# Optimization experiments

Hardware: AMD Instinct MI355X
Metric: run time of the kernel (lower is better)

The kernel has to match this reference:

```python
import jax, jax.numpy as jnp
import numpy as np

N = 50000      # nodes
E = 800000     # edges
D_IN = 512
D_OUT = 512
EDGE_DIM = 3


def setup_inputs() -> dict:
    key = jax.random.key(0)
    k = jax.random.split(key, 6)
    x = jax.random.normal(k[0], (N, D_IN), dtype=jnp.float32)
    edge_index = jax.random.randint(k[1], (2, E), 0, N, dtype=jnp.int64)
    edge_attr = jax.random.normal(k[2], (E, EDGE_DIM), dtype=jnp.float32)
    # xavier-uniform-ish init for linear weights
    lim1 = (6.0 / (D_IN + D_OUT)) ** 0.5
    lin_w = jax.random.uniform(k[3], (D_OUT, D_IN), minval=-lim1, maxval=lim1, dtype=jnp.float32)
    lin_b = jnp.zeros((D_OUT,), dtype=jnp.float32)
    lim2 = (6.0 / (EDGE_DIM + 1)) ** 0.5
    conf_w = jax.random.uniform(k[4], (1, EDGE_DIM), minval=-lim2, maxval=lim2, dtype=jnp.float32)
    conf_b = jnp.zeros((1,), dtype=jnp.float32)
    return {"x": x, "edge_index": edge_index, "edge_attr": edge_attr,
            "lin_w": lin_w, "lin_b": lin_b, "conf_w": conf_w, "conf_b": conf_b}


def reference(x, edge_index, edge_attr, lin_w, lin_b, conf_w, conf_b):
    row, col = edge_index[0], edge_index[1]
    # edge confidence weight: sigmoid(conf_lin(edge_attr)) -> [E]
    edge_weight = jax.nn.sigmoid(edge_attr @ conf_w.T + conf_b)[:, 0]
    # degree of source nodes (count of row occurrences), inverse sqrt with inf/nan -> 0
    deg = jnp.zeros((x.shape[0],), dtype=x.dtype).at[row].add(1.0)
    deg_safe = jnp.where(deg > 0, deg, 1.0)
    deg_inv_sqrt = jnp.where(deg > 0, jax.lax.rsqrt(deg_safe), 0.0)
    norm = deg_inv_sqrt[row] * deg_inv_sqrt[col] * edge_weight  # [E]
    norm = jnp.where(jnp.isnan(norm), 0.0, norm)
    # gather-scale-scatter: out[col] += x[row] * norm
    out = jnp.zeros_like(x).at[col].add(x[row] * norm[:, None])
    return out @ lin_w.T + lin_b
```

## Files before the change

### kernel.cpp

```cpp
#include <hip/hip_runtime.h>

#define NDIM 512

typedef __bf16 bf16x8 __attribute__((ext_vector_type(8)));
typedef float  f32x4  __attribute__((ext_vector_type(4)));

__device__ inline ushort f2bf(float f) {
    uint b = __float_as_uint(f);
    return (ushort)((b + 0x7fffu + ((b >> 16) & 1u)) >> 16);
}
__device__ inline float bflo(uint u) { return __uint_as_float(u << 16); }
__device__ inline float bfhi(uint u) { return __uint_as_float(u & 0xffff0000u); }
__device__ inline uint packbf(float lo, float hi) {
    return ((uint)f2bf(hi) << 16) | (uint)f2bf(lo);
}

__device__ inline void gload16(const ushort* g, ushort* l) {
    __builtin_amdgcn_global_load_lds(
        (const __attribute__((address_space(1))) uint*)g,
        (__attribute__((address_space(3))) uint*)l, 16, 0, 0);
}

__global__ __launch_bounds__(256) void f2bf_kernel(const float* __restrict__ in,
                                                   ushort* __restrict__ out, int n4) {
    int i = blockIdx.x * 256 + threadIdx.x;
    if (i >= n4) return;
    float4 v = ((const float4*)in)[i];
    ushort4 o;
    o.x = f2bf(v.x); o.y = f2bf(v.y); o.z = f2bf(v.z); o.w = f2bf(v.w);
    ((ushort4*)out)[i] = o;
}

__global__ __launch_bounds__(256) void hist_kernel(const int* __restrict__ ei,
                                                   int* __restrict__ deg_row,
                                                   int* __restrict__ cnt_col, int E) {
    int e = blockIdx.x * 256 + threadIdx.x;
    if (e < E) {
        atomicAdd(&deg_row[ei[e]], 1);
        atomicAdd(&cnt_col[ei[E + e]], 1);
    }
}

__global__ __launch_bounds__(256) void rsqrt_kernel(const int* __restrict__ deg,
                                                    float* __restrict__ dis, int n) {
    int i = blockIdx.x * 256 + threadIdx.x;
    if (i < n) {
        int d = deg[i];
        dis[i] = (d > 0) ? rsqrtf((float)d) : 0.0f;
    }
}

__global__ __launch_bounds__(1024) void scan_kernel(const int* __restrict__ cnt,
                                                    int* __restrict__ base, int n) {
    __shared__ int wsum[16];
    __shared__ int carry_s;
    int tid = threadIdx.x;
    int lane = tid & 63, wid = tid >> 6;
    if (tid == 0) carry_s = 0;
    __syncthreads();
    for (int s = 0; s < n; s += 4096) {
        int i0 = s + tid * 4;
        int v0 = 0, v1 = 0, v2 = 0, v3 = 0;
        if (i0 + 3 < n) {
            int4 q = *(const int4*)(cnt + i0);
            v0 = q.x; v1 = q.y; v2 = q.z; v3 = q.w;
        } else if (i0 < n) {
            v0 = cnt[i0];
            if (i0 + 1 < n) v1 = cnt[i0 + 1];
            if (i0 + 2 < n) v2 = cnt[i0 + 2];
        }
        int tsum = v0 + v1 + v2 + v3;
        int incl = tsum;
#pragma unroll
        for (int off = 1; off < 64; off <<= 1) {
            int t = __shfl_up(incl, off, 64);
            if (lane >= off) incl += t;
        }
        if (lane == 63) wsum[wid] = incl;
        __syncthreads();
        int add = carry_s;
#pragma unroll
        for (int w = 0; w < 16; ++w) if (w < wid) add += wsum[w];
        int run = add + incl - tsum;
        if (i0 + 0 < n) base[i0 + 0] = run; run += v0;
        if (i0 + 1 < n) base[i0 + 1] = run; run += v1;
        if (i0 + 2 < n) base[i0 + 2] = run; run += v2;
        if (i0 + 3 < n) base[i0 + 3] = run;
        __syncthreads();
        if (tid == 1023) carry_s = add + incl;
        __syncthreads();
    }
    if (tid == 0) base[n] = carry_s;
}

__global__ __launch_bounds__(256) void fill_kernel(
        const int* __restrict__ ei, const float* __restrict__ ea,
        const float* __restrict__ dis,
        const float* __restrict__ conf_w, const float* __restrict__ conf_b,
        const int* __restrict__ base, int* __restrict__ fill_cnt,
        int2* __restrict__ rn_sorted, int E) {
    int e = blockIdx.x * 256 + threadIdx.x;
    if (e >= E) return;
    int row = ei[e];
    int col = ei[E + e];
    float w = ea[(size_t)e*3+0]*conf_w[0] + ea[(size_t)e*3+1]*conf_w[1]
            + ea[(size_t)e*3+2]*conf_w[2] + conf_b[0];
    w = 1.0f / (1.0f + __expf(-w));
    float nm = dis[row] * dis[col] * w;
    int pos = base[col] + atomicAdd(&fill_cnt[col], 1);
    rn_sorted[pos] = make_int2(row, __float_as_int(nm));
}

__global__ __launch_bounds__(256) void agg_kernel(
        const ushort* __restrict__ xh, const int2* __restrict__ rn,
        const int* __restrict__ base, ushort* __restrict__ aggh, int N) {
    int wid  = threadIdx.x >> 6;
    int lane = threadIdx.x & 63;
    int node = blockIdx.x * 4 + wid;
    if (node >= N) return;
    int start = base[node], end = base[node + 1];
    const ushort* xc = xh + lane * 8;
    float a0 = 0.f, a1 = 0.f, a2 = 0.f, a3 = 0.f;
    float a4 = 0.f, a5 = 0.f, a6 = 0.f, a7 = 0.f;
    int p = start;
    for (; p + 4 <= end; p += 4) {
        int2 e0 = rn[p + 0];
        int2 e1 = rn[p + 1];
        int2 e2 = rn[p + 2];
        int2 e3 = rn[p + 3];
        uint4 u0 = *(const uint4*)(xc + ((size_t)e0.x << 9));
        uint4 u1 = *(const uint4*)(xc + ((size_t)e1.x << 9));
        uint4 u2 = *(const uint4*)(xc + ((size_t)e2.x << 9));
        uint4 u3 = *(const uint4*)(xc + ((size_t)e3.x << 9));
        float n0 = __int_as_float(e0.y);
        float n1 = __int_as_float(e1.y);
        float n2 = __int_as_float(e2.y);
        float n3 = __int_as_float(e3.y);
        a0 = fmaf(bflo(u0.x), n0, a0); a1 = fmaf(bfhi(u0.x), n0, a1);
        a2 = fmaf(bflo(u0.y), n0, a2); a3 = fmaf(bfhi(u0.y), n0, a3);
        a4 = fmaf(bflo(u0.z), n0, a4); a5 = fmaf(bfhi(u0.z), n0, a5);
        a6 = fmaf(bflo(u0.w), n0, a6); a7 = fmaf(bfhi(u0.w), n0, a7);
        a0 = fmaf(bflo(u1.x), n1, a0); a1 = fmaf(bfhi(u1.x), n1, a1);
        a2 = fmaf(bflo(u1.y), n1, a2); a3 = fmaf(bfhi(u1.y), n1, a3);
        a4 = fmaf(bflo(u1.z), n1, a4); a5 = fmaf(bfhi(u1.z), n1, a5);
        a6 = fmaf(bflo(u1.w), n1, a6); a7 = fmaf(bfhi(u1.w), n1, a7);
        a0 = fmaf(bflo(u2.x), n2, a0); a1 = fmaf(bfhi(u2.x), n2, a1);
        a2 = fmaf(bflo(u2.y), n2, a2); a3 = fmaf(bfhi(u2.y), n2, a3);
        a4 = fmaf(bflo(u2.z), n2, a4); a5 = fmaf(bfhi(u2.z), n2, a5);
        a6 = fmaf(bflo(u2.w), n2, a6); a7 = fmaf(bfhi(u2.w), n2, a7);
        a0 = fmaf(bflo(u3.x), n3, a0); a1 = fmaf(bfhi(u3.x), n3, a1);
        a2 = fmaf(bflo(u3.y), n3, a2); a3 = fmaf(bfhi(u3.y), n3, a3);
        a4 = fmaf(bflo(u3.z), n3, a4); a5 = fmaf(bfhi(u3.z), n3, a5);
        a6 = fmaf(bflo(u3.w), n3, a6); a7 = fmaf(bfhi(u3.w), n3, a7);
    }
    for (; p < end; ++p) {
        int2 e = rn[p];
        uint4 u = *(const uint4*)(xc + ((size_t)e.x << 9));
        float nm = __int_as_float(e.y);
        a0 = fmaf(bflo(u.x), nm, a0); a1 = fmaf(bfhi(u.x), nm, a1);
        a2 = fmaf(bflo(u.y), nm, a2); a3 = fmaf(bfhi(u.y), nm, a3);
        a4 = fmaf(bflo(u.z), nm, a4); a5 = fmaf(bfhi(u.z), nm, a5);
        a6 = fmaf(bflo(u.w), nm, a6); a7 = fmaf(bfhi(u.w), nm, a7);
    }
    uint4 o;
    o.x = packbf(a0, a1);
    o.y = packbf(a2, a3);
    o.z = packbf(a4, a5);
    o.w = packbf(a6, a7);
    *(uint4*)(aggh + (size_t)node * NDIM + lane * 8) = o;
}

__global__ __launch_bounds__(256) void mfma_gemm(
        const ushort* __restrict__ A,
        const ushort* __restrict__ B,
        const float* __restrict__ bias,
        float* __restrict__ out, int M) {
    __shared__ ushort As[128 * 32];
    __shared__ ushort Bs[128 * 32];
    int m0 = blockIdx.x * 128;
    int n0 = blockIdx.y * 128;
    int tid  = threadIdx.x;
    int lane = tid & 63;
    int wave = tid >> 6;
    int wr = wave >> 1, wc = wave & 1;
    int quad = lane >> 4, l16 = lane & 15;
    int lrow = lane >> 2, lcol = (lane & 3) << 3;

    f32x4 acc[4][4] = {};

    for (int k0 = 0; k0 < NDIM; k0 += 32) {
#pragma unroll
        for (int i = 0; i < 2; ++i) {
            int ch = wave * 2 + i;
            int r  = ch * 16 + lrow;
            int gm = m0 + r; if (gm >= M) gm = M - 1;
            gload16(A + ((size_t)gm << 9) + k0 + lcol, &As[ch * 512]);
            gload16(B + ((size_t)(n0 + r) << 9) + k0 + lcol, &Bs[ch * 512]);
        }
        __syncthreads();
#pragma unroll
        for (int mt = 0; mt < 4; ++mt) {
            bf16x8 a = *(const bf16x8*)&As[(wr * 64 + mt * 16 + l16) * 32 + quad * 8];
#pragma unroll
            for (int nt = 0; nt < 4; ++nt) {
                bf16x8 b = *(const bf16x8*)&Bs[(wc * 64 + nt * 16 + l16) * 32 + quad * 8];
                acc[mt][nt] = __builtin_amdgcn_mfma_f32_16x16x32_bf16(a, b, acc[mt][nt], 0, 0, 0);
            }
        }
        __syncthreads();
    }
#pragma unroll
    for (int mt = 0; mt < 4; ++mt) {
#pragma unroll
        for (int nt = 0; nt < 4; ++nt) {
            int gn = n0 + wc * 64 + nt * 16 + l16;
            float bv = bias[gn];
#pragma unroll
            for (int r = 0; r < 4; ++r) {
                int gm = m0 + wr * 64 + mt * 16 + quad * 4 + r;
                if (gm < M) out[(size_t)gm * NDIM + gn] = acc[mt][nt][r] + bv;
            }
        }
    }
}

extern "C" void kernel_launch(void* const* d_in, const int* in_sizes, int n_in,
                              void* d_out, int out_size, void* d_ws, size_t ws_size,
                              hipStream_t stream) {
    const float* x      = (const float*)d_in[0];
    const int*   ei     = (const int*)  d_in[1];
    const float* ea     = (const float*)d_in[2];
    const float* lin_w  = (const float*)d_in[3];
    const float* lin_b  = (const float*)d_in[4];
    const float* conf_w = (const float*)d_in[5];
    const float* conf_b = (const float*)d_in[6];
    float* out = (float*)d_out;

    int N = in_sizes[0] / NDIM;
    int E = in_sizes[2] / 3;

    char* p = (char*)d_ws;
    auto alloc = [&](size_t bytes) {
        char* q = p;
        p += (bytes + 255) & ~(size_t)255;
        return q;
    };
    ushort* aggh       = (ushort*)alloc((size_t)N * NDIM * sizeof(ushort));
    ushort* wh         = (ushort*)alloc((size_t)NDIM * NDIM * sizeof(ushort));
    int*   deg_row     = (int*)  alloc((size_t)N * sizeof(int));
    int*   cnt_col     = (int*)  alloc((size_t)N * sizeof(int));
    int*   fill_cnt    = (int*)  alloc((size_t)N * sizeof(int));
    float* dis         = (float*)alloc((size_t)N * sizeof(float));
    int*   base        = (int*)  alloc((size_t)(N + 1) * sizeof(int));
    int2*  rn_sorted   = (int2*) alloc((size_t)E * sizeof(int2));

    ushort* xh = (ushort*)d_out;

    size_t zero_bytes = (size_t)((char*)dis - (char*)deg_row);
    (void)hipMemsetAsync(deg_row, 0, zero_bytes, stream);

    int gE = (E + 255) / 256;
    int gN = (N + 255) / 256;
    int x4 = (N * NDIM) / 4, w4 = (NDIM * NDIM) / 4;
    f2bf_kernel  <<<(x4 + 255) / 256, 256, 0, stream>>>(x, xh, x4);
    f2bf_kernel  <<<(w4 + 255) / 256, 256, 0, stream>>>(lin_w, wh, w4);
    hist_kernel  <<<gE, 256, 0, stream>>>(ei, deg_row, cnt_col, E);
    rsqrt_kernel <<<gN, 256, 0, stream>>>(deg_row, dis, N);
    scan_kernel  <<<1, 1024, 0, stream>>>(cnt_col, base, N);
    fill_kernel  <<<gE, 256, 0, stream>>>(ei, ea, dis, conf_w, conf_b,
                                          base, fill_cnt, rn_sorted, E);
    agg_kernel   <<<(N + 3) / 4, 256, 0, stream>>>(xh, rn_sorted, base, aggh, N);
    dim3 g((N + 127) / 128, NDIM / 128);
    mfma_gemm    <<<g, 256, 0, stream>>>(aggh, wh, lin_b, out, N);
}
```

Baseline: 500.4 us.

## Pad CSR segments to multiples of 8, software-pipeline aggregation, swizzle GEMM blocks

```diff
diff --git a/kernel.cpp b/kernel.cpp
--- a/kernel.cpp
+++ b/kernel.cpp
@@ -51,7 +51,8 @@
 }
 
 __global__ __launch_bounds__(1024) void scan_kernel(const int* __restrict__ cnt,
-                                                    int* __restrict__ base, int n) {
+                                                    int* __restrict__ base,
+                                                    int* __restrict__ fc, int n) {
     __shared__ int wsum[16];
     __shared__ int carry_s;
     int tid = threadIdx.x;
@@ -69,6 +70,8 @@
             if (i0 + 1 < n) v1 = cnt[i0 + 1];
             if (i0 + 2 < n) v2 = cnt[i0 + 2];
         }
+        v0 = (v0 + 7) & ~7; v1 = (v1 + 7) & ~7;
+        v2 = (v2 + 7) & ~7; v3 = (v3 + 7) & ~7;
         int tsum = v0 + v1 + v2 + v3;
         int incl = tsum;
 #pragma unroll
@@ -82,10 +85,10 @@
 #pragma unroll
         for (int w = 0; w < 16; ++w) if (w < wid) add += wsum[w];
         int run = add + incl - tsum;
-        if (i0 + 0 < n) base[i0 + 0] = run; run += v0;
-        if (i0 + 1 < n) base[i0 + 1] = run; run += v1;
-        if (i0 + 2 < n) base[i0 + 2] = run; run += v2;
-        if (i0 + 3 < n) base[i0 + 3] = run;
+        if (i0 + 0 < n) { base[i0 + 0] = run; fc[i0 + 0] = run; } run += v0;
+        if (i0 + 1 < n) { base[i0 + 1] = run; fc[i0 + 1] = run; } run += v1;
+        if (i0 + 2 < n) { base[i0 + 2] = run; fc[i0 + 2] = run; } run += v2;
+        if (i0 + 3 < n) { base[i0 + 3] = run; fc[i0 + 3] = run; }
         __syncthreads();
         if (tid == 1023) carry_s = add + incl;
         __syncthreads();
@@ -97,8 +100,7 @@
         const int* __restrict__ ei, const float* __restrict__ ea,
         const float* __restrict__ dis,
         const float* __restrict__ conf_w, const float* __restrict__ conf_b,
-        const int* __restrict__ base, int* __restrict__ fill_cnt,
-        int2* __restrict__ rn_sorted, int E) {
+        int* __restrict__ fill_cnt, int2* __restrict__ rn_sorted, int E) {
     int e = blockIdx.x * 256 + threadIdx.x;
     if (e >= E) return;
     int row = ei[e];
@@ -107,9 +109,15 @@
             + ea[(size_t)e*3+2]*conf_w[2] + conf_b[0];
     w = 1.0f / (1.0f + __expf(-w));
     float nm = dis[row] * dis[col] * w;
-    int pos = base[col] + atomicAdd(&fill_cnt[col], 1);
+    int pos = atomicAdd(&fill_cnt[col], 1);
     rn_sorted[pos] = make_int2(row, __float_as_int(nm));
 }
+
+#define ACC8(u, nm)                                                     \
+    a0 = fmaf(bflo((u).x), (nm), a0); a1 = fmaf(bfhi((u).x), (nm), a1); \
+    a2 = fmaf(bflo((u).y), (nm), a2); a3 = fmaf(bfhi((u).y), (nm), a3); \
+    a4 = fmaf(bflo((u).z), (nm), a4); a5 = fmaf(bfhi((u).z), (nm), a5); \
+    a6 = fmaf(bflo((u).w), (nm), a6); a7 = fmaf(bfhi((u).w), (nm), a7);
 
 __global__ __launch_bounds__(256) void agg_kernel(
         const ushort* __restrict__ xh, const int2* __restrict__ rn,
@@ -123,44 +131,32 @@
     float a0 = 0.f, a1 = 0.f, a2 = 0.f, a3 = 0.f;
     float a4 = 0.f, a5 = 0.f, a6 = 0.f, a7 = 0.f;
     int p = start;
-    for (; p + 4 <= end; p += 4) {
-        int2 e0 = rn[p + 0];
-        int2 e1 = rn[p + 1];
-        int2 e2 = rn[p + 2];
-        int2 e3 = rn[p + 3];
-        uint4 u0 = *(const uint4*)(xc + ((size_t)e0.x << 9));
-        uint4 u1 = *(const uint4*)(xc + ((size_t)e1.x << 9));
-        uint4 u2 = *(const uint4*)(xc + ((size_t)e2.x << 9));
-        uint4 u3 = *(const uint4*)(xc + ((size_t)e3.x << 9));
-        float n0 = __int_as_float(e0.y);
-        float n1 = __int_as_float(e1.y);
-        float n2 = __int_as_float(e2.y);
-        float n3 = __int_as_float(e3.y);
-        a0 = fmaf(bflo(u0.x), n0, a0); a1 = fmaf(bfhi(u0.x), n0, a1);
-        a2 = fmaf(bflo(u0.y), n0, a2); a3 = fmaf(bfhi(u0.y), n0, a3);
-        a4 = fmaf(bflo(u0.z), n0, a4); a5 = fmaf(bfhi(u0.z), n0, a5);
-        a6 = fmaf(bflo(u0.w), n0, a6); a7 = fmaf(bfhi(u0.w), n0, a7);
-        a0 = fmaf(bflo(u1.x), n1, a0); a1 = fmaf(bfhi(u1.x), n1, a1);
-        a2 = fmaf(bflo(u1.y), n1, a2); a3 = fmaf(bfhi(u1.y), n1, a3);
-        a4 = fmaf(bflo(u1.z), n1, a4); a5 = fmaf(bfhi(u1.z), n1, a5);
-        a6 = fmaf(bflo(u1.w), n1, a6); a7 = fmaf(bfhi(u1.w), n1, a7);
-        a0 = fmaf(bflo(u2.x), n2, a0); a1 = fmaf(bfhi(u2.x), n2, a1);
-        a2 = fmaf(bflo(u2.y), n2, a2); a3 = fmaf(bfhi(u2.y), n2, a3);
-        a4 = fmaf(bflo(u2.z), n2, a4); a5 = fmaf(bfhi(u2.z), n2, a5);
-        a6 = fmaf(bflo(u2.w), n2, a6); a7 = fmaf(bfhi(u2.w), n2, a7);
-        a0 = fmaf(bflo(u3.x), n3, a0); a1 = fmaf(bfhi(u3.x), n3, a1);
-        a2 = fmaf(bflo(u3.y), n3, a2); a3 = fmaf(bfhi(u3.y), n3, a3);
-        a4 = fmaf(bflo(u3.z), n3, a4); a5 = fmaf(bfhi(u3.z), n3, a5);
-        a6 = fmaf(bflo(u3.w), n3, a6); a7 = fmaf(bfhi(u3.w), n3, a7);
-    }
-    for (; p < end; ++p) {
-        int2 e = rn[p];
-        uint4 u = *(const uint4*)(xc + ((size_t)e.x << 9));
-        float nm = __int_as_float(e.y);
-        a0 = fmaf(bflo(u.x), nm, a0); a1 = fmaf(bfhi(u.x), nm, a1);
-        a2 = fmaf(bflo(u.y), nm, a2); a3 = fmaf(bfhi(u.y), nm, a3);
-        a4 = fmaf(bflo(u.z), nm, a4); a5 = fmaf(bfhi(u.z), nm, a5);
-        a6 = fmaf(bflo(u.w), nm, a6); a7 = fmaf(bfhi(u.w), nm, a7);
+    if (p < end) {
+        int2 e0 = rn[p+0], e1 = rn[p+1], e2 = rn[p+2], e3 = rn[p+3];
+        int2 e4 = rn[p+4], e5 = rn[p+5], e6 = rn[p+6], e7 = rn[p+7];
+        for (;;) {
+            uint4 u0 = *(const uint4*)(xc + ((size_t)e0.x << 9));
+            uint4 u1 = *(const uint4*)(xc + ((size_t)e1.x << 9));
+            uint4 u2 = *(const uint4*)(xc + ((size_t)e2.x << 9));
+            uint4 u3 = *(const uint4*)(xc + ((size_t)e3.x << 9));
+            uint4 u4 = *(const uint4*)(xc + ((size_t)e4.x << 9));
+            uint4 u5 = *(const uint4*)(xc + ((size_t)e5.x << 9));
+            uint4 u6 = *(const uint4*)(xc + ((size_t)e6.x << 9));
+            uint4 u7 = *(const uint4*)(xc + ((size_t)e7.x << 9));
+            p += 8;
+            int q = (p < end) ? p : start;
+            int2 f0 = rn[q+0], f1 = rn[q+1], f2 = rn[q+2], f3 = rn[q+3];
+            int2 f4 = rn[q+4], f5 = rn[q+5], f6 = rn[q+6], f7 = rn[q+7];
+            float n0 = __int_as_float(e0.y), n1 = __int_as_float(e1.y);
+            float n2 = __int_as_float(e2.y), n3 = __int_as_float(e3.y);
+            float n4 = __int_as_float(e4.y), n5 = __int_as_float(e5.y);
+            float n6 = __int_as_float(e6.y), n7 = __int_as_float(e7.y);
+            ACC8(u0, n0); ACC8(u1, n1); ACC8(u2, n2); ACC8(u3, n3);
+            ACC8(u4, n4); ACC8(u5, n5); ACC8(u6, n6); ACC8(u7, n7);
+            if (p >= end) break;
+            e0 = f0; e1 = f1; e2 = f2; e3 = f3;
+            e4 = f4; e5 = f5; e6 = f6; e7 = f7;
+        }
     }
     uint4 o;
     o.x = packbf(a0, a1);
@@ -177,8 +173,21 @@
         float* __restrict__ out, int M) {
     __shared__ ushort As[128 * 32];
     __shared__ ushort Bs[128 * 32];
-    int m0 = blockIdx.x * 128;
-    int n0 = blockIdx.y * 128;
+    int Mb = (M + 127) >> 7;
+    int lin = blockIdx.x;
+    int full = (Mb >> 3) << 5;
+    int mb, nb;
+    if (lin < full) {
+        mb = ((lin >> 5) << 3) + (lin & 7);
+        nb = (lin >> 3) & 3;
+    } else {
+        int r = lin - full;
+        int mrem = Mb & 7;
+        mb = ((Mb >> 3) << 3) + (r % mrem);
+        nb = r / mrem;
+    }
+    int m0 = mb << 7;
+    int n0 = nb << 7;
     int tid  = threadIdx.x;
     int lane = tid & 63;
     int wave = tid >> 6;
@@ -252,11 +261,12 @@
     int*   fill_cnt    = (int*)  alloc((size_t)N * sizeof(int));
     float* dis         = (float*)alloc((size_t)N * sizeof(float));
     int*   base        = (int*)  alloc((size_t)(N + 1) * sizeof(int));
-    int2*  rn_sorted   = (int2*) alloc((size_t)E * sizeof(int2));
+    size_t rn_cap      = (size_t)E + 7 * (size_t)N + 8;
+    int2*  rn_sorted   = (int2*) alloc(rn_cap * sizeof(int2));
 
     ushort* xh = (ushort*)d_out;
 
-    size_t zero_bytes = (size_t)((char*)dis - (char*)deg_row);
+    size_t zero_bytes = (size_t)((char*)(rn_sorted + rn_cap) - (char*)deg_row);
     (void)hipMemsetAsync(deg_row, 0, zero_bytes, stream);
 
     int gE = (E + 255) / 256;
@@ -266,10 +276,10 @@
     f2bf_kernel  <<<(w4 + 255) / 256, 256, 0, stream>>>(lin_w, wh, w4);
     hist_kernel  <<<gE, 256, 0, stream>>>(ei, deg_row, cnt_col, E);
     rsqrt_kernel <<<gN, 256, 0, stream>>>(deg_row, dis, N);
-    scan_kernel  <<<1, 1024, 0, stream>>>(cnt_col, base, N);
+    scan_kernel  <<<1, 1024, 0, stream>>>(cnt_col, base, fill_cnt, N);
     fill_kernel  <<<gE, 256, 0, stream>>>(ei, ea, dis, conf_w, conf_b,
-                                          base, fill_cnt, rn_sorted, E);
+                                          fill_cnt, rn_sorted, E);
     agg_kernel   <<<(N + 3) / 4, 256, 0, stream>>>(xh, rn_sorted, base, aggh, N);
-    dim3 g((N + 127) / 128, NDIM / 128);
-    mfma_gemm    <<<g, 256, 0, stream>>>(aggh, wh, lin_b, out, N);
-}
+    int Mb = (N + 127) >> 7;
+    mfma_gemm    <<<Mb * 4, 256, 0, stream>>>(aggh, wh, lin_b, out, N);
+}
```

Measured after the change: 504.9 us. Within noise of the previous version (+0.9%).
